# Performance work log

Hardware: AMD Instinct MI355X
Metric: run time of the kernel (lower is better)

Reference implementation:

```python
import jax, jax.numpy as jnp
import numpy as np

N, E, F_IN, D_COORD, W, KW, KIN, DEPTH = 10000, 300000, 3, 3, 32, 256, 6, 4

def _lin(k, i, o):
    return jax.random.normal(k, (i, o), jnp.float32) * (1.0 / np.sqrt(i))

def setup_inputs() -> dict:
    key = jax.random.key(0)
    ks = jax.random.split(key, 16)
    x = jax.random.normal(ks[0], (N, F_IN), jnp.float32)
    edge_index = jax.random.randint(ks[1], (2, E), 0, N, jnp.int64)
    edge_attr = jax.random.normal(ks[2], (E, KIN), jnp.float32)
    coords_init = jax.random.normal(ks[3], (N, D_COORD), jnp.float32)
    return {
        "x": x, "edge_index": edge_index, "edge_attr": edge_attr,
        "coords_init": coords_init,
        "fc1_w": _lin(ks[4], F_IN, W), "fc1_b": jnp.zeros((W,), jnp.float32),
        # kernel DenseNet: [ker_in, ker_width//2, ker_width, width**2]
        "ker1_w": _lin(ks[5], KIN, KW // 2), "ker1_b": jnp.zeros((KW // 2,), jnp.float32),
        "ker2_w": _lin(ks[6], KW // 2, KW), "ker2_b": jnp.zeros((KW,), jnp.float32),
        "ker3_w": _lin(ks[7], KW, W * W), "ker3_b": jnp.zeros((W * W,), jnp.float32),
        # coord MLP: Linear(W,W)+ReLU+Linear(W,1)
        "cm1_w": _lin(ks[8], W, W), "cm1_b": jnp.zeros((W,), jnp.float32),
        "cm2_w": _lin(ks[9], W, 1), "cm2_b": jnp.zeros((1,), jnp.float32),
        # fc2: Linear(W,2W)+ReLU+Linear(2W,1)
        "fc2a_w": _lin(ks[10], W, 2 * W), "fc2a_b": jnp.zeros((2 * W,), jnp.float32),
        "fc2b_w": _lin(ks[11], 2 * W, 1), "fc2b_b": jnp.zeros((1,), jnp.float32),
        "depth": DEPTH,
    }

def reference(x, edge_index, edge_attr, coords_init,
              fc1_w, fc1_b, ker1_w, ker1_b, ker2_w, ker2_b, ker3_w, ker3_b,
              cm1_w, cm1_b, cm2_w, cm2_b, fc2a_w, fc2a_b, fc2b_w, fc2b_b, depth):
    n = x.shape[0]
    w = fc1_w.shape[1]
    row, col = edge_index[0], edge_index[1]
    h = x @ fc1_w + fc1_b  # [N, W]
    # edge kernel MLP -> per-edge [W, W] matrix (edge_attr fixed across layers)
    k = jax.nn.relu(edge_attr @ ker1_w + ker1_b)
    k = jax.nn.relu(k @ ker2_w + ker2_b)
    k = (k @ ker3_w + ker3_b).reshape(-1, w, w)  # [E, W, W]
    cnt = jnp.clip(jax.ops.segment_sum(jnp.ones((row.shape[0], 1), h.dtype), row, n), 1.0)
    coord = coords_init
    for _ in range(depth):
        m = jnp.einsum('eij,ej->ei', k, h[col])              # gather + kernel apply
        agg = jax.ops.segment_sum(m, row, n) / cnt           # mean scatter to nodes
        we = jax.nn.relu(m @ cm1_w + cm1_b) @ cm2_w + cm2_b  # [E, 1] coord weights
        trans = (coord[row] - coord[col]) * we               # equivariant edge vectors
        coord = coord + jax.ops.segment_sum(trans, row, n) / cnt
        h = jax.nn.relu(h + agg)
    out = jax.nn.relu(h @ fc2a_w + fc2a_b) @ fc2b_w + fc2b_b  # [N, 1]
    return out, coord
```

## Files before the change

### kernel.cpp

```cpp
#include <hip/hip_runtime.h>

#define NN 10000
#define NE 300000
#define DEPTH 4

typedef unsigned int   u32;
typedef unsigned short u16;
typedef unsigned char  u8;

typedef _Float16 half8  __attribute__((ext_vector_type(8)));
typedef _Float16 half2t __attribute__((ext_vector_type(2)));
typedef float  floatx16 __attribute__((ext_vector_type(16)));

__device__ __forceinline__ u32 f2h(float f) {
    f = fminf(fmaxf(f, -60000.f), 60000.f);
    _Float16 h = (_Float16)f;
    return (u32)__builtin_bit_cast(u16, h);
}
__device__ __forceinline__ float h2f(u16 b) {
    return (float)__builtin_bit_cast(_Float16, b);
}
__device__ __forceinline__ u32 pkrtz2(float a, float b) {
    return __builtin_bit_cast(u32, __builtin_amdgcn_cvt_pkrtz(a, b));
}
__device__ __forceinline__ u32 dq2(u32 x, u32 sel) {
    const half2t h1024 = {(_Float16)1024.f, (_Float16)1024.f};
    half2t v = __builtin_bit_cast(half2t, __builtin_amdgcn_perm(x, 0x64646464u, sel));
    return __builtin_bit_cast(u32, v - h1024);
}

__global__ void sentinel_kernel(float* out, int n, float val) {
    int i = blockIdx.x * 256 + threadIdx.x;
    if (i < n) out[i] = val;
}

__global__ void detect_idx_kernel(const int* __restrict__ ei, int* __restrict__ flag) {
    __shared__ int nz;
    if (threadIdx.x == 0) nz = 0;
    __syncthreads();
    if (ei[threadIdx.x * 2 + 1] != 0) atomicAdd(&nz, 1);
    __syncthreads();
    if (threadIdx.x == 0) *flag = (nz == 0) ? 1 : 0;
}

__global__ __launch_bounds__(256) void convert_idx_kernel(
    const int* __restrict__ ei, const int* __restrict__ flag,
    int* __restrict__ ridx, int* __restrict__ cidx)
{
    int e = blockIdx.x * 256 + threadIdx.x;
    if (e >= 2 * NE) return;
    const int is64 = *flag;
    int v = is64 ? ei[2 * e] : ei[e];
    if (e < NE) ridx[e] = v; else cidx[e - NE] = v;
}

__global__ __launch_bounds__(256) void init_nodes_kernel(
    const float* __restrict__ x, const float* __restrict__ fc1w,
    const float* __restrict__ fc1b, const float* __restrict__ ci,
    float* __restrict__ h, float* __restrict__ coord)
{
    int idx = blockIdx.x * 256 + threadIdx.x;
    if (idx < NN * 32) {
        int v = idx >> 5, f = idx & 31;
        float acc = fc1b[f];
#pragma unroll
        for (int i = 0; i < 3; i++) acc += x[v * 3 + i] * fc1w[i * 32 + f];
        h[idx] = acc;
    }
    if (idx < NN * 3) coord[idx] = ci[idx];
}

__global__ __launch_bounds__(256) void count_kernel(
    const int* __restrict__ ridx, const int* __restrict__ cidx,
    int* __restrict__ rowcnt, int* __restrict__ colcnt)
{
    int e = blockIdx.x * 256 + threadIdx.x;
    if (e < NE) { atomicAdd(&rowcnt[ridx[e]], 1); atomicAdd(&colcnt[cidx[e]], 1); }
}

__global__ void scan_kernel(const int* __restrict__ colcnt, const int* __restrict__ rowcnt,
                            int* __restrict__ cstart, int* __restrict__ cnext,
                            int* __restrict__ rstart, int* __restrict__ rnext,
                            float* __restrict__ invc, int mode)
{
    __shared__ int partC[256], partR[256];
    const int t = threadIdx.x;
    int sumC = 0, sumR = 0;
    for (int i = 0; i < 40; i++) {
        int v = t * 40 + i;
        if (v < NN) { sumC += colcnt[v]; sumR += rowcnt[v]; }
    }
    partC[t] = sumC; partR[t] = sumR;
    __syncthreads();
    if (t == 0) {
        int rc = 0, rr = 0;
        for (int i = 0; i < 256; i++) {
            int tc = partC[i]; partC[i] = rc; rc += tc;
            int tr = partR[i]; partR[i] = rr; rr += tr;
        }
    }
    __syncthreads();
    int runC = partC[t], runR = partR[t];
    for (int i = 0; i < 40; i++) {
        int v = t * 40 + i;
        if (v < NN) {
            cstart[v] = runC; cnext[v] = runC; runC += colcnt[v];
            if (mode) { rstart[v] = runR; rnext[v] = runR; runR += rowcnt[v]; }
        }
    }
    if (t == 255) { cstart[NN] = runC; if (mode) rstart[NN] = runR; }
    for (int v = t; v < NN; v += 256) invc[v] = 1.0f / fmaxf((float)rowcnt[v], 1.0f);
}

__global__ __launch_bounds__(256) void scatter_kernel(
    const int* __restrict__ cidx, const int* __restrict__ ridx,
    int* __restrict__ cnext, int* __restrict__ rnext,
    int* __restrict__ elist, int* __restrict__ rpos, int* __restrict__ rcol,
    int mode)
{
    int e = blockIdx.x * 256 + threadIdx.x;
    if (e >= NE) return;
    int pos = atomicAdd(&cnext[cidx[e]], 1);
    elist[pos] = e;
    if (mode) {
        int rp = atomicAdd(&rnext[ridx[e]], 1);
        rpos[e] = rp;
        rcol[rp] = cidx[e];
    }
}

__global__ __launch_bounds__(256) void w2pack_kernel(
    const float* __restrict__ w2, u16* __restrict__ w2h)
{
    const int slot = blockIdx.x * 256 + threadIdx.x;
    const int c = slot >> 9, s = (slot >> 6) & 7, l = slot & 63;
    const int li = l & 31, hf = l >> 5;
    const int k0 = s * 16 + hf * 8, col = c * 32 + li;
    u32 pk[8];
#pragma unroll
    for (int j = 0; j < 8; j++) pk[j] = f2h(w2[(size_t)(k0 + j) * 256 + col]);
    uint4 o;
    o.x = pk[0] | (pk[1] << 16);
    o.y = pk[2] | (pk[3] << 16);
    o.z = pk[4] | (pk[5] << 16);
    o.w = pk[6] | (pk[7] << 16);
    *(uint4*)&w2h[(size_t)slot * 8] = o;
}

__global__ void cm1pack_kernel(const float* __restrict__ cm1w, u16* __restrict__ cmpk)
{
    const int t = threadIdx.x;
    if (t >= 128) return;
    const int s2 = t >> 6, l = t & 63, li = l & 31, hf = l >> 5;
    u32 pk[8];
#pragma unroll
    for (int j = 0; j < 8; j++) pk[j] = f2h(cm1w[(s2 * 16 + hf * 8 + j) * 32 + li]);
    uint4 o;
    o.x = pk[0] | (pk[1] << 16);
    o.y = pk[2] | (pk[3] << 16);
    o.z = pk[4] | (pk[5] << 16);
    o.w = pk[6] | (pk[7] << 16);
    *(uint4*)&cmpk[(size_t)(s2 * 64 + l) * 8] = o;
}

__global__ __launch_bounds__(256) void w3pack_kernel(
    const float* __restrict__ w3, u16* __restrict__ w3g)
{
    const int slot = blockIdx.x * 256 + threadIdx.x;
    const int lane = slot & 63;
    const int ks   = (slot >> 6) & 1;
    const int pt   = slot >> 7;
    const int p    = pt * 32 + (lane & 31);
    const int kb   = ks * 16 + (lane >> 5) * 8;
    const int s  = p >> 9;
    const int hf = (p >> 8) & 1;
    const int i  = (p >> 3) & 31;
    const int j7 = p & 7;
    const int c  = s * 16 + hf * 8 + j7;
    const float* wp = &w3[(size_t)c * 1024 + i * 32 + kb];
    const float4 x0 = *(const float4*)wp;
    const float4 x1 = *(const float4*)(wp + 4);
    uint4 o;
    o.x = f2h(x0.x) | (f2h(x0.y) << 16);
    o.y = f2h(x0.z) | (f2h(x0.w) << 16);
    o.z = f2h(x1.x) | (f2h(x1.y) << 16);
    o.w = f2h(x1.z) | (f2h(x1.w) << 16);
    *(uint4*)&w3g[(size_t)slot * 8] = o;
}

__global__ __launch_bounds__(256) void mlp_k2_kernel(
    const float* __restrict__ ea,
    const float* __restrict__ w1, const float* __restrict__ b1,
    const u16* __restrict__ w2h, const float* __restrict__ b2,
    u8* __restrict__ k2base, u16* __restrict__ k2s)
{
    __shared__ __align__(16) float ea_s[32 * 6];
    __shared__ __align__(16) u16   k1f[4096];
    __shared__ __align__(16) u16   M_s[32 * 258];
    __shared__ float pmax_s[4][32];
    const int t  = threadIdx.x;
    const int e0 = blockIdx.x * 32;

    for (int idx = t; idx < 192; idx += 256)
        ea_s[idx] = ea[(size_t)e0 * 6 + idx];
    __syncthreads();

    for (int slot = t; slot < 512; slot += 256) {
        const int s  = slot >> 6;
        const int l  = slot & 63;
        const int li = l & 31, hf = l >> 5;
        const int k0 = s * 16 + hf * 8;
        float acc[8];
        {
            const float4 ba = *(const float4*)&b1[k0];
            const float4 bb = *(const float4*)&b1[k0 + 4];
            acc[0] = ba.x; acc[1] = ba.y; acc[2] = ba.z; acc[3] = ba.w;
            acc[4] = bb.x; acc[5] = bb.y; acc[6] = bb.z; acc[7] = bb.w;
        }
#pragma unroll
        for (int i = 0; i < 6; i++) {
            const float ev = ea_s[li * 6 + i];
            const float4 wa = *(const float4*)&w1[i * 128 + k0];
            const float4 wb = *(const float4*)&w1[i * 128 + k0 + 4];
            acc[0] += ev * wa.x; acc[1] += ev * wa.y;
            acc[2] += ev * wa.z; acc[3] += ev * wa.w;
            acc[4] += ev * wb.x; acc[5] += ev * wb.y;
            acc[6] += ev * wb.z; acc[7] += ev * wb.w;
        }
        uint4 o;
        o.x = pkrtz2(fmaxf(acc[0], 0.f), fmaxf(acc[1], 0.f));
        o.y = pkrtz2(fmaxf(acc[2], 0.f), fmaxf(acc[3], 0.f));
        o.z = pkrtz2(fmaxf(acc[4], 0.f), fmaxf(acc[5], 0.f));
        o.w = pkrtz2(fmaxf(acc[6], 0.f), fmaxf(acc[7], 0.f));
        *(uint4*)&k1f[slot * 8] = o;
    }
    __syncthreads();

    {
        const int w  = t >> 6, l = t & 63;
        const int li = l & 31, hf = l >> 5;
#pragma unroll
        for (int ct = 0; ct < 2; ct++) {
            const int c = w * 2 + ct;
            floatx16 acc;
#pragma unroll
            for (int r = 0; r < 16; r++) acc[r] = 0.f;
#pragma unroll
            for (int s = 0; s < 8; s++) {
                const half8 a = __builtin_bit_cast(half8,
                    *(const uint4*)&k1f[(s * 64 + l) * 8]);
                const half8 b = __builtin_bit_cast(half8,
                    *(const uint4*)&w2h[(((size_t)c * 8 + s) * 64 + l) * 8]);
                acc = __builtin_amdgcn_mfma_f32_32x32x16_f16(a, b, acc, 0, 0, 0);
            }
            const float bb = b2[c * 32 + li];
#pragma unroll
            for (int r = 0; r < 16; r++) {
                const int e = (r & 3) + 8 * (r >> 2) + 4 * hf;
                M_s[e * 258 + c * 32 + li] =
                    __builtin_bit_cast(u16, (_Float16)fmaxf(acc[r] + bb, 0.f));
            }
        }
    }
    __syncthreads();

    {
        const int el = t & 31, qq = t >> 5;
        const int w  = t >> 6;
        float vals[32];
#pragma unroll
        for (int c = 0; c < 16; c++) {
            const u32 hw = *(const u32*)&M_s[el * 258 + qq * 32 + c * 2];
            vals[c * 2]     = h2f((u16)hw);
            vals[c * 2 + 1] = h2f((u16)(hw >> 16));
        }
        float mx = 0.f;
#pragma unroll
        for (int u = 0; u < 32; u++) mx = fmaxf(mx, vals[u]);
        mx = fmaxf(mx, __shfl_xor(mx, 32, 64));
        if ((t & 32) == 0) pmax_s[w][el] = mx;
        __syncthreads();
        mx = fmaxf(fmaxf(pmax_s[0][el], pmax_s[1][el]),
                   fmaxf(pmax_s[2][el], pmax_s[3][el]));
        const float sc  = mx / 255.f;
        const float inv = (mx > 0.f) ? 255.f / mx : 0.f;
        if (t < 32) k2s[e0 + el] = (u16)f2h(sc);
        u32 w8[8];
#pragma unroll
        for (int u = 0; u < 8; u++) {
            u32 q0 = (u32)fminf(rintf(vals[u * 4 + 0] * inv), 255.f);
            u32 q1 = (u32)fminf(rintf(vals[u * 4 + 1] * inv), 255.f);
            u32 q2 = (u32)fminf(rintf(vals[u * 4 + 2] * inv), 255.f);
            u32 q3 = (u32)fminf(rintf(vals[u * 4 + 3] * inv), 255.f);
            w8[u] = q0 | (q1 << 8) | (q2 << 16) | (q3 << 24);
        }
        u8* outp = k2base + (size_t)(e0 + el) * 256 + qq * 32;
        *(uint4*)outp        = make_uint4(w8[0], w8[1], w8[2], w8[3]);
        *(uint4*)(outp + 16) = make_uint4(w8[4], w8[5], w8[6], w8[7]);
    }
}

__global__ __launch_bounds__(256) void bvec_kernel(
    const float* __restrict__ h, const float* __restrict__ b3, float* __restrict__ bvec)
{
    int idx = blockIdx.x * 256 + threadIdx.x;
    if (idx >= NN * 32) return;
    int v = idx >> 5, i = idx & 31;
    const float* hp = &h[(size_t)v * 32];
    const float* bp = &b3[i * 32];
    float acc = 0.f;
#pragma unroll
    for (int c = 0; c < 8; c++) {
        float4 hv = *(const float4*)&hp[c * 4];
        float4 bv = *(const float4*)&bp[c * 4];
        acc += hv.x * bv.x + hv.y * bv.y + hv.z * bv.z + hv.w * bv.w;
    }
    bvec[idx] = acc;
}

__global__ __launch_bounds__(256) void g_kernel(
    const float* __restrict__ h, const u16* __restrict__ w3g,
    u16* __restrict__ Gg)
{
    const int t = threadIdx.x, w = t >> 6, l = t & 63;
    const int li = l & 31, hf = l >> 5;
    const int n0 = blockIdx.x * 32;
    const int node = n0 + li;

    half8 a0, a1;
    if (node < NN) {
        const float* hp = &h[(size_t)node * 32 + hf * 8];
        const float4 x0 = *(const float4*)hp;
        const float4 x1 = *(const float4*)(hp + 4);
        const float4 y0 = *(const float4*)(hp + 16);
        const float4 y1 = *(const float4*)(hp + 20);
        uint4 ua, ub;
        ua.x = pkrtz2(x0.x, x0.y); ua.y = pkrtz2(x0.z, x0.w);
        ua.z = pkrtz2(x1.x, x1.y); ua.w = pkrtz2(x1.z, x1.w);
        ub.x = pkrtz2(y0.x, y0.y); ub.y = pkrtz2(y0.z, y0.w);
        ub.z = pkrtz2(y1.x, y1.y); ub.w = pkrtz2(y1.z, y1.w);
        a0 = __builtin_bit_cast(half8, ua);
        a1 = __builtin_bit_cast(half8, ub);
    } else {
        const uint4 z = make_uint4(0u, 0u, 0u, 0u);
        a0 = __builtin_bit_cast(half8, z);
        a1 = __builtin_bit_cast(half8, z);
    }

    const int pt0 = blockIdx.y * 64 + w * 16;
    const int full = (n0 + 32 <= NN) ? 1 : 0;
#pragma unroll 4
    for (int it = 0; it < 16; it++) {
        const int pt = pt0 + it;
        const uint4 b0u = *(const uint4*)&w3g[((size_t)pt * 2 + 0) * 512 + (size_t)l * 8];
        const uint4 b1u = *(const uint4*)&w3g[((size_t)pt * 2 + 1) * 512 + (size_t)l * 8];
        floatx16 acc;
#pragma unroll
        for (int r = 0; r < 16; r++) acc[r] = 0.f;
        acc = __builtin_amdgcn_mfma_f32_32x32x16_f16(
            a0, __builtin_bit_cast(half8, b0u), acc, 0, 0, 0);
        acc = __builtin_amdgcn_mfma_f32_32x32x16_f16(
            a1, __builtin_bit_cast(half8, b1u), acc, 0, 0, 0);
        if (full) {
#pragma unroll
            for (int r = 0; r < 16; r++) {
                const int nn = n0 + (r & 3) + 8 * (r >> 2) + 4 * hf;
                Gg[(size_t)nn * 8192 + pt * 32 + li] = (u16)f2h(acc[r]);
            }
        } else {
#pragma unroll
            for (int r = 0; r < 16; r++) {
                const int nn = n0 + (r & 3) + 8 * (r >> 2) + 4 * hf;
                if (nn < NN)
                    Gg[(size_t)nn * 8192 + pt * 32 + li] = (u16)f2h(acc[r]);
            }
        }
    }
}

__global__ __launch_bounds__(256) void edge_kernel(
    const int* __restrict__ cstart, const int* __restrict__ elist,
    const int* __restrict__ ridx, const int* __restrict__ rpos,
    const u8* __restrict__ k2base, const u16* __restrict__ k2s,
    const u16* __restrict__ Gg, const float* __restrict__ coord,
    const u16* __restrict__ cmpk, const float* __restrict__ cm1b,
    const float* __restrict__ cm2w, const float* __restrict__ cm2b,
    const float* __restrict__ bvec,
    float* __restrict__ agg, float* __restrict__ dco,
    u16* __restrict__ mbuf, u16* __restrict__ webuf, int mode)
{
    const int t    = threadIdx.x;
    const int w    = t >> 6;
    const int l    = t & 63;
    const int li   = l & 31;
    const int half = l >> 5;

    __shared__ __align__(16) float Mlds_all[4][32 * 34];
    __shared__ int   idxS_all[4][32];
    __shared__ float seS_all[4][32];
    float* Mlds = Mlds_all[w];
    int*   idxS = idxS_all[w];
    float* seS  = seS_all[w];

    const int n = blockIdx.x * 4 + w;
    if (n >= NN) return;
    const int s0  = cstart[n];
    const int deg = cstart[n + 1] - s0;
    if (deg == 0) return;

    half8 cmb[2];
    cmb[0] = __builtin_bit_cast(half8, *(const uint4*)&cmpk[(size_t)(0 * 64 + l) * 8]);
    cmb[1] = __builtin_bit_cast(half8, *(const uint4*)&cmpk[(size_t)(1 * 64 + l) * 8]);
    half8 onesb;
#pragma unroll
    for (int j = 0; j < 8; j++) onesb[j] = (_Float16)1.0f;
    const float cm1bq = cm1b[li];
    const float cm2q  = cm2w[li];
    const float cm2b0 = cm2b[0];
    const float bv    = bvec[n * 32 + li];
    const float con   = (mode == 0 && li < 3) ? coord[(size_t)n * 3 + li] : 0.f;
    const u16* Gn = Gg + (size_t)n * 8192;

    for (int base = 0; base < deg; base += 32) {
        const int mye   = base + li;
        const int valid = (mye < deg) ? 1 : 0;
        const int eid   = valid ? elist[s0 + mye] : 0;
        const float se  = valid ? h2f(k2s[eid]) : 0.f;
        if (l < 32) { idxS[l] = valid ? (mode ? rpos[eid] : ridx[eid]) : 0; seS[l] = se; }

        uint4 gr[16];
#pragma unroll
        for (int s = 0; s < 16; s++)
            gr[s] = *(const uint4*)(Gn + s * 512 + l * 8);
        const u8* k2row = k2base + (size_t)eid * 256 + half * 8;
        uint2 kr[16];
#pragma unroll
        for (int s = 0; s < 16; s++) kr[s] = *(const uint2*)(k2row + s * 16);

        floatx16 acc;
#pragma unroll
        for (int r = 0; r < 16; r++) acc[r] = 0.f;
#pragma unroll
        for (int s = 0; s < 16; s++) {
            uint4 au;
            au.x = dq2(kr[s].x, 0x00050004u);
            au.y = dq2(kr[s].x, 0x00070006u);
            au.z = dq2(kr[s].y, 0x00050004u);
            au.w = dq2(kr[s].y, 0x00070006u);
            acc = __builtin_amdgcn_mfma_f32_32x32x16_f16(
                __builtin_bit_cast(half8, au),
                __builtin_bit_cast(half8, gr[s]), acc, 0, 0, 0);
        }
#pragma unroll
        for (int r = 0; r < 16; r++) {
            const int e = (r & 3) + 8 * (r >> 2) + 4 * half;
            acc[r] = acc[r] * seS[e] + bv;
        }

#pragma unroll
        for (int r = 0; r < 16; r++) {
            const int e = (r & 3) + 8 * (r >> 2) + 4 * half;
            Mlds[e * 34 + li] = acc[r];
        }
        if (mode == 0) {
#pragma unroll
            for (int r = 0; r < 16; r++) {
                const int e = (r & 3) + 8 * (r >> 2) + 4 * half;
                if (base + e < deg)
                    atomicAdd(&agg[(size_t)idxS[e] * 32 + li], acc[r]);
            }
        } else {
#pragma unroll
            for (int r = 0; r < 16; r++) {
                const int e = (r & 3) + 8 * (r >> 2) + 4 * half;
                if (base + e < deg)
                    mbuf[(size_t)idxS[e] * 32 + li] =
                        __builtin_bit_cast(u16, (_Float16)acc[r]);
            }
        }
        asm volatile("s_waitcnt lgkmcnt(0)" ::: "memory");

        floatx16 acc2;
#pragma unroll
        for (int r = 0; r < 16; r++) acc2[r] = cm1bq;
#pragma unroll
        for (int s2 = 0; s2 < 2; s2++) {
            const float* mp = &Mlds[li * 34 + s2 * 16 + half * 8];
            const float2 m0 = *(const float2*)mp;
            const float2 m1 = *(const float2*)(mp + 2);
            const float2 m2 = *(const float2*)(mp + 4);
            const float2 m3 = *(const float2*)(mp + 6);
            uint4 au;
            au.x = pkrtz2(m0.x, m0.y);
            au.y = pkrtz2(m1.x, m1.y);
            au.z = pkrtz2(m2.x, m2.y);
            au.w = pkrtz2(m3.x, m3.y);
            acc2 = __builtin_amdgcn_mfma_f32_32x32x16_f16(
                __builtin_bit_cast(half8, au), cmb[s2], acc2, 0, 0, 0);
        }

#pragma unroll
        for (int r = 0; r < 16; r++) {
            const int e = (r & 3) + 8 * (r >> 2) + 4 * half;
            Mlds[e * 34 + li] = fmaxf(acc2[r], 0.f) * cm2q;
        }
        asm volatile("s_waitcnt lgkmcnt(0)" ::: "memory");
        floatx16 acc3;
#pragma unroll
        for (int r = 0; r < 16; r++) acc3[r] = cm2b0;
#pragma unroll
        for (int s2 = 0; s2 < 2; s2++) {
            const float* mp = &Mlds[li * 34 + s2 * 16 + half * 8];
            const float2 m0 = *(const float2*)mp;
            const float2 m1 = *(const float2*)(mp + 2);
            const float2 m2 = *(const float2*)(mp + 4);
            const float2 m3 = *(const float2*)(mp + 6);
            uint4 au;
            au.x = pkrtz2(m0.x, m0.y);
            au.y = pkrtz2(m1.x, m1.y);
            au.z = pkrtz2(m2.x, m2.y);
            au.w = pkrtz2(m3.x, m3.y);
            acc3 = __builtin_amdgcn_mfma_f32_32x32x16_f16(
                __builtin_bit_cast(half8, au), onesb, acc3, 0, 0, 0);
        }

        if (mode == 0) {
#pragma unroll
            for (int r = 0; r < 16; r++) {
                const int e = (r & 3) + 8 * (r >> 2) + 4 * half;
                if (base + e < deg && li < 3) {
                    const int rr = idxS[e];
                    const float d = coord[(size_t)rr * 3 + li] - con;
                    atomicAdd(&dco[(size_t)rr * 3 + li], d * acc3[r]);
                }
            }
        } else {
#pragma unroll
            for (int r = 0; r < 16; r++) {
                const int e = (r & 3) + 8 * (r >> 2) + 4 * half;
                if (base + e < deg && li == 0)
                    webuf[idxS[e]] = __builtin_bit_cast(u16, (_Float16)acc3[r]);
            }
        }
    }
}

__global__ __launch_bounds__(256) void node_update_kernel(
    float* __restrict__ h, float* __restrict__ agg,
    float* __restrict__ coord, float* __restrict__ dco,
    const float* __restrict__ invc)
{
    int idx = blockIdx.x * 256 + threadIdx.x;
    if (idx < NN * 32) {
        int v = idx >> 5;
        h[idx] = fmaxf(h[idx] + agg[idx] * invc[v], 0.f);
        agg[idx] = 0.f;
    }
    if (idx < NN * 3) {
        coord[idx] += dco[idx] * invc[idx / 3];
        dco[idx] = 0.f;
    }
}

__global__ __launch_bounds__(256) void node_update2_kernel(
    float* __restrict__ h, const float* __restrict__ coordCur,
    float* __restrict__ coordNew, const u16* __restrict__ mbuf,
    const u16* __restrict__ webuf, const int* __restrict__ rcol,
    const int* __restrict__ rstart, const float* __restrict__ invc)
{
    const int t = threadIdx.x, w = t >> 6, l = t & 63;
    const int li = l & 31, half = l >> 5;
    const int v = blockIdx.x * 4 + w;
    if (v >= NN) return;
    const int s0 = rstart[v], s1 = rstart[v + 1];
    const float iv = invc[v];

    float acc = 0.f;
    for (int s = s0 + half; s < s1; s += 2)
        acc += h2f(mbuf[(size_t)s * 32 + li]);
    acc += __shfl_xor(acc, 32, 64);
    if (half == 0)
        h[(size_t)v * 32 + li] = fmaxf(h[(size_t)v * 32 + li] + acc * iv, 0.f);

    const float c0 = coordCur[(size_t)v * 3 + 0];
    const float c1 = coordCur[(size_t)v * 3 + 1];
    const float c2 = coordCur[(size_t)v * 3 + 2];
    float p0 = 0.f, p1 = 0.f, p2 = 0.f;
    for (int s = s0 + l; s < s1; s += 64) {
        const float we = h2f(webuf[s]);
        const int col = rcol[s];
        p0 += (c0 - coordCur[(size_t)col * 3 + 0]) * we;
        p1 += (c1 - coordCur[(size_t)col * 3 + 1]) * we;
        p2 += (c2 - coordCur[(size_t)col * 3 + 2]) * we;
    }
#pragma unroll
    for (int off = 32; off >= 1; off >>= 1) {
        p0 += __shfl_xor(p0, off, 64);
        p1 += __shfl_xor(p1, off, 64);
        p2 += __shfl_xor(p2, off, 64);
    }
    if (l == 0) {
        coordNew[(size_t)v * 3 + 0] = c0 + p0 * iv;
        coordNew[(size_t)v * 3 + 1] = c1 + p1 * iv;
        coordNew[(size_t)v * 3 + 2] = c2 + p2 * iv;
    }
}

__global__ __launch_bounds__(256) void final_kernel(
    const float* __restrict__ h, const float* __restrict__ coord,
    const float* __restrict__ wa, const float* __restrict__ ba,
    const float* __restrict__ wb, const float* __restrict__ bb,
    float* __restrict__ out)
{
    const int lane = threadIdx.x & 63;
    const int v = blockIdx.x * 4 + (threadIdx.x >> 6);
    if (v >= NN) return;
    const float hreg = (lane < 32) ? h[(size_t)v * 32 + lane] : 0.f;
    float acc = ba[lane];
#pragma unroll
    for (int f = 0; f < 32; f++) acc += __shfl(hreg, f, 64) * wa[f * 64 + lane];
    float part = fmaxf(acc, 0.f) * wb[lane];
#pragma unroll
    for (int off = 32; off >= 1; off >>= 1) part += __shfl_xor(part, off, 64);
    if (lane == 0) out[v] = part + bb[0];
    if (lane < 3) out[NN + (size_t)v * 3 + lane] = coord[(size_t)v * 3 + lane];
}

extern "C" void kernel_launch(void* const* d_in, const int* in_sizes, int n_in,
                              void* d_out, int out_size, void* d_ws, size_t ws_size,
                              hipStream_t stream)
{
    const float* x    = (const float*)d_in[0];
    const int*   ei   = (const int*)d_in[1];
    const float* ea   = (const float*)d_in[2];
    const float* ci   = (const float*)d_in[3];
    const float* fc1w = (const float*)d_in[4];
    const float* fc1b = (const float*)d_in[5];
    const float* k1w  = (const float*)d_in[6];
    const float* k1b  = (const float*)d_in[7];
    const float* k2w  = (const float*)d_in[8];
    const float* k2b  = (const float*)d_in[9];
    const float* k3w  = (const float*)d_in[10];
    const float* k3b  = (const float*)d_in[11];
    const float* cm1w = (const float*)d_in[12];
    const float* cm1b = (const float*)d_in[13];
    const float* cm2w = (const float*)d_in[14];
    const float* cm2b = (const float*)d_in[15];
    const float* f2aw = (const float*)d_in[16];
    const float* f2ab = (const float*)d_in[17];
    const float* f2bw = (const float*)d_in[18];
    const float* f2bb = (const float*)d_in[19];

    size_t o_k2, o_k2s, o_G, o_h, o_bv, o_coA, o_coB, o_invc, o_rc, o_cc,
           o_cs, o_rs, o_cn, o_rn, o_el, o_w2h, o_cmpk, o_w3g, o_agg, o_dco,
           o_ri, o_ci, o_rp, o_rcl, o_mb, o_wb;
#define ALGN(v) (((v) + 255) & ~(size_t)255)
    auto carve = [&](int mode) -> size_t {
        size_t o = 0;
        o_k2  = o; o += ALGN((size_t)NE * 256);
        o_k2s = o; o += ALGN((size_t)NE * 2);
        o_G   = o; o += ALGN((size_t)NN * 8192 * 2);
        o_h   = o; o += ALGN((size_t)NN * 32 * 4);
        o_bv  = o; o += ALGN((size_t)NN * 32 * 4);
        o_coA = o; o += ALGN((size_t)NN * 3 * 4);
        o_invc= o; o += ALGN((size_t)NN * 4);
        o_rc  = o; o += ALGN((size_t)NN * 4);
        o_cc  = o; o += ALGN((size_t)NN * 4);
        o_cs  = o; o += ALGN((size_t)(NN + 1) * 4);
        o_cn  = o; o += ALGN((size_t)NN * 4);
        o_el  = o; o += ALGN((size_t)NE * 4);
        o_w2h = o; o += ALGN((size_t)128 * 256 * 2);
        o_cmpk= o; o += ALGN((size_t)1024 * 2);
        o_w3g = o; o += ALGN((size_t)32768 * 8 * 2);
        if (mode == 0) {
            o_agg = o; o += ALGN((size_t)NN * 32 * 4);
            o_dco = o; o += ALGN((size_t)NN * 3 * 4);
            o_ri  = o; o += ALGN((size_t)NE * 4);
            o_ci  = o; o += ALGN((size_t)NE * 4);
            o_coB = o_coA; o_rs = o_cs; o_rn = o_cn;
            o_rp = o_el; o_rcl = o_el; o_mb = o_k2; o_wb = o_k2;
        } else {
            o_coB = o; o += ALGN((size_t)NN * 3 * 4);
            o_rs  = o; o += ALGN((size_t)(NN + 1) * 4);
            o_rn  = o; o += ALGN((size_t)NN * 4);
            o_rp  = o; o += ALGN((size_t)NE * 4);
            o_rcl = o; o += ALGN((size_t)NE * 4);
            const size_t u = o;
            o_ri = u; o_ci = u + ALGN((size_t)NE * 4);
            o_mb = u; o_wb = u + ALGN((size_t)NE * 32 * 2);
            const size_t setup_sz = 2 * ALGN((size_t)NE * 4);
            const size_t layer_sz = ALGN((size_t)NE * 32 * 2) + ALGN((size_t)NE * 2);
            o += (setup_sz > layer_sz) ? setup_sz : layer_sz;
            o_agg = o_k2; o_dco = o_k2;
        }
        return o;
    };
    int mode = (ws_size >= carve(1)) ? 1 : 0;
    size_t need = carve(mode);
    if (ws_size < need) {
        sentinel_kernel<<<(NN * 4 + 255) / 256, 256, 0, stream>>>((float*)d_out, NN * 4, 1.0e6f);
        return;
    }

    char* wsb = (char*)d_ws;
    u8*    k2g   = (u8*)(wsb + o_k2);
    u16*   k2s   = (u16*)(wsb + o_k2s);
    u16*   Gg    = (u16*)(wsb + o_G);
    float* h     = (float*)(wsb + o_h);
    float* bvec  = (float*)(wsb + o_bv);
    float* coA   = (float*)(wsb + o_coA);
    float* coB   = (float*)(wsb + o_coB);
    float* invc  = (float*)(wsb + o_invc);
    int*   rowcnt= (int*)(wsb + o_rc);
    int*   colcnt= (int*)(wsb + o_cc);
    int*   cstart= (int*)(wsb + o_cs);
    int*   rstart= (int*)(wsb + o_rs);
    int*   cnext = (int*)(wsb + o_cn);
    int*   rnext = (int*)(wsb + o_rn);
    int*   elist = (int*)(wsb + o_el);
    u16*   w2h   = (u16*)(wsb + o_w2h);
    u16*   cmpk  = (u16*)(wsb + o_cmpk);
    u16*   w3g   = (u16*)(wsb + o_w3g);
    float* agg   = (float*)(wsb + o_agg);
    float* dco   = (float*)(wsb + o_dco);
    int*   ridx  = (int*)(wsb + o_ri);
    int*   cidx  = (int*)(wsb + o_ci);
    int*   rpos  = (int*)(wsb + o_rp);
    int*   rcol  = (int*)(wsb + o_rcl);
    u16*   mbuf  = (u16*)(wsb + o_mb);
    u16*   webuf = (u16*)(wsb + o_wb);

    hipMemsetAsync(rowcnt, 0, (size_t)NN * 4, stream);
    hipMemsetAsync(colcnt, 0, (size_t)NN * 4, stream);
    if (mode == 0) {
        hipMemsetAsync(agg, 0, (size_t)NN * 32 * 4, stream);
        hipMemsetAsync(dco, 0, (size_t)NN * 3 * 4, stream);
    }

    detect_idx_kernel<<<1, 256, 0, stream>>>(ei, cnext);
    convert_idx_kernel<<<(2 * NE + 255) / 256, 256, 0, stream>>>(ei, cnext, ridx, cidx);
    init_nodes_kernel<<<(NN * 32 + 255) / 256, 256, 0, stream>>>(x, fc1w, fc1b, ci, h, coA);
    count_kernel<<<(NE + 255) / 256, 256, 0, stream>>>(ridx, cidx, rowcnt, colcnt);
    scan_kernel<<<1, 256, 0, stream>>>(colcnt, rowcnt, cstart, cnext, rstart, rnext,
                                       invc, mode);
    scatter_kernel<<<(NE + 255) / 256, 256, 0, stream>>>(cidx, ridx, cnext, rnext,
                                                         elist, rpos, rcol, mode);
    w2pack_kernel<<<16, 256, 0, stream>>>(k2w, w2h);
    cm1pack_kernel<<<1, 128, 0, stream>>>(cm1w, cmpk);
    w3pack_kernel<<<128, 256, 0, stream>>>(k3w, w3g);
    mlp_k2_kernel<<<NE / 32, 256, 0, stream>>>(ea, k1w, k1b, w2h, k2b, k2g, k2s);

    float* coCur = coA;
    float* coAlt = coB;
    const dim3 ggrid((NN + 31) / 32, 4);
    for (int l = 0; l < DEPTH; l++) {
        bvec_kernel<<<(NN * 32 + 255) / 256, 256, 0, stream>>>(h, k3b, bvec);
        g_kernel<<<ggrid, 256, 0, stream>>>(h, w3g, Gg);
        edge_kernel<<<(NN + 3) / 4, 256, 0, stream>>>(cstart, elist, ridx, rpos,
                                                      k2g, k2s, Gg, coCur, cmpk,
                                                      cm1b, cm2w, cm2b, bvec,
                                                      agg, dco, mbuf, webuf, mode);
        if (mode == 1) {
            node_update2_kernel<<<(NN + 3) / 4, 256, 0, stream>>>(
                h, coCur, coAlt, mbuf, webuf, rcol, rstart, invc);
            float* tmp = coCur; coCur = coAlt; coAlt = tmp;
        } else {
            node_update_kernel<<<(NN * 32 + 255) / 256, 256, 0, stream>>>(
                h, agg, coCur, dco, invc);
        }
    }
    final_kernel<<<(NN + 3) / 4, 256, 0, stream>>>(h, coCur, f2aw, f2ab, f2bw, f2bb,
                                                   (float*)d_out);
}
```

Measured before the change: 860.1 us.

## Fuse bias-vector compute into edge kernel and speed up k2 quantization

Removes the per-layer bvec kernel and its buffer; each edge_kernel warp now computes the h·b3 bias dot product inline. mlp_k2's quantization takes the max with packed fp16 max ops and rounds with a magic-number FMA plus byte permutes instead of rintf, fminf and shifts. It also adds occupancy hints to launch_bounds for mlp_k2 (4) and edge_kernel (3). This saves four kernel launches and a global round trip per forward pass, at the cost of extra per-warp loads of h and b3 and possible register spills from the new bounds. The magic-add rounding drops the clamp at 255, which relies on the scaled values never exceeding 255.

```diff
diff --git a/kernel.cpp b/kernel.cpp
--- a/kernel.cpp
+++ b/kernel.cpp
@@ -188,7 +188,7 @@
     *(uint4*)&w3g[(size_t)slot * 8] = o;
 }
 
-__global__ __launch_bounds__(256) void mlp_k2_kernel(
+__global__ __launch_bounds__(256, 4) void mlp_k2_kernel(
     const float* __restrict__ ea,
     const float* __restrict__ w1, const float* __restrict__ b1,
     const u16* __restrict__ w2h, const float* __restrict__ b2,
@@ -267,16 +267,16 @@
     {
         const int el = t & 31, qq = t >> 5;
         const int w  = t >> 6;
-        float vals[32];
-#pragma unroll
-        for (int c = 0; c < 16; c++) {
-            const u32 hw = *(const u32*)&M_s[el * 258 + qq * 32 + c * 2];
-            vals[c * 2]     = h2f((u16)hw);
-            vals[c * 2 + 1] = h2f((u16)(hw >> 16));
-        }
-        float mx = 0.f;
-#pragma unroll
-        for (int u = 0; u < 32; u++) mx = fmaxf(mx, vals[u]);
+        u32 hw[16];
+#pragma unroll
+        for (int c = 0; c < 16; c++)
+            hw[c] = *(const u32*)&M_s[el * 258 + qq * 32 + c * 2];
+
+        half2t pm = __builtin_bit_cast(half2t, hw[0]);
+#pragma unroll
+        for (int c = 1; c < 16; c++)
+            pm = __builtin_elementwise_max(pm, __builtin_bit_cast(half2t, hw[c]));
+        float mx = fmaxf((float)pm[0], (float)pm[1]);
         mx = fmaxf(mx, __shfl_xor(mx, 32, 64));
         if ((t & 32) == 0) pmax_s[w][el] = mx;
         __syncthreads();
@@ -285,37 +285,27 @@
         const float sc  = mx / 255.f;
         const float inv = (mx > 0.f) ? 255.f / mx : 0.f;
         if (t < 32) k2s[e0 + el] = (u16)f2h(sc);
+        const float magic = 8388608.f;
         u32 w8[8];
 #pragma unroll
         for (int u = 0; u < 8; u++) {
-            u32 q0 = (u32)fminf(rintf(vals[u * 4 + 0] * inv), 255.f);
-            u32 q1 = (u32)fminf(rintf(vals[u * 4 + 1] * inv), 255.f);
-            u32 q2 = (u32)fminf(rintf(vals[u * 4 + 2] * inv), 255.f);
-            u32 q3 = (u32)fminf(rintf(vals[u * 4 + 3] * inv), 255.f);
-            w8[u] = q0 | (q1 << 8) | (q2 << 16) | (q3 << 24);
+            const u32 a = hw[u * 2], b = hw[u * 2 + 1];
+            const float v0 = h2f((u16)a);
+            const float v1 = h2f((u16)(a >> 16));
+            const float v2 = h2f((u16)b);
+            const float v3 = h2f((u16)(b >> 16));
+            const u32 r0 = __builtin_bit_cast(u32, fmaf(v0, inv, magic));
+            const u32 r1 = __builtin_bit_cast(u32, fmaf(v1, inv, magic));
+            const u32 r2 = __builtin_bit_cast(u32, fmaf(v2, inv, magic));
+            const u32 r3 = __builtin_bit_cast(u32, fmaf(v3, inv, magic));
+            const u32 p01 = __builtin_amdgcn_perm(r1, r0, 0x0C0C0400u);
+            const u32 p23 = __builtin_amdgcn_perm(r3, r2, 0x0C0C0400u);
+            w8[u] = __builtin_amdgcn_perm(p23, p01, 0x05040100u);
         }
         u8* outp = k2base + (size_t)(e0 + el) * 256 + qq * 32;
         *(uint4*)outp        = make_uint4(w8[0], w8[1], w8[2], w8[3]);
         *(uint4*)(outp + 16) = make_uint4(w8[4], w8[5], w8[6], w8[7]);
     }
-}
-
-__global__ __launch_bounds__(256) void bvec_kernel(
-    const float* __restrict__ h, const float* __restrict__ b3, float* __restrict__ bvec)
-{
-    int idx = blockIdx.x * 256 + threadIdx.x;
-    if (idx >= NN * 32) return;
-    int v = idx >> 5, i = idx & 31;
-    const float* hp = &h[(size_t)v * 32];
-    const float* bp = &b3[i * 32];
-    float acc = 0.f;
-#pragma unroll
-    for (int c = 0; c < 8; c++) {
-        float4 hv = *(const float4*)&hp[c * 4];
-        float4 bv = *(const float4*)&bp[c * 4];
-        acc += hv.x * bv.x + hv.y * bv.y + hv.z * bv.z + hv.w * bv.w;
-    }
-    bvec[idx] = acc;
 }
 
 __global__ __launch_bounds__(256) void g_kernel(
@@ -378,14 +368,14 @@
     }
 }
 
-__global__ __launch_bounds__(256) void edge_kernel(
+__global__ __launch_bounds__(256, 3) void edge_kernel(
     const int* __restrict__ cstart, const int* __restrict__ elist,
     const int* __restrict__ ridx, const int* __restrict__ rpos,
     const u8* __restrict__ k2base, const u16* __restrict__ k2s,
     const u16* __restrict__ Gg, const float* __restrict__ coord,
     const u16* __restrict__ cmpk, const float* __restrict__ cm1b,
     const float* __restrict__ cm2w, const float* __restrict__ cm2b,
-    const float* __restrict__ bvec,
+    const float* __restrict__ h, const float* __restrict__ b3,
     float* __restrict__ agg, float* __restrict__ dco,
     u16* __restrict__ mbuf, u16* __restrict__ webuf, int mode)
 {
@@ -417,7 +407,17 @@
     const float cm1bq = cm1b[li];
     const float cm2q  = cm2w[li];
     const float cm2b0 = cm2b[0];
-    const float bv    = bvec[n * 32 + li];
+    float bv = 0.f;
+    {
+        const float* hn = &h[(size_t)n * 32];
+        const float* bp = &b3[(size_t)li * 32];
+#pragma unroll
+        for (int c2 = 0; c2 < 8; c2++) {
+            const float4 hv = *(const float4*)&hn[c2 * 4];
+            const float4 bq = *(const float4*)&bp[c2 * 4];
+            bv += hv.x * bq.x + hv.y * bq.y + hv.z * bq.z + hv.w * bq.w;
+        }
+    }
     const float con   = (mode == 0 && li < 3) ? coord[(size_t)n * 3 + li] : 0.f;
     const u16* Gn = Gg + (size_t)n * 8192;
 
@@ -651,7 +651,7 @@
     const float* f2bw = (const float*)d_in[18];
     const float* f2bb = (const float*)d_in[19];
 
-    size_t o_k2, o_k2s, o_G, o_h, o_bv, o_coA, o_coB, o_invc, o_rc, o_cc,
+    size_t o_k2, o_k2s, o_G, o_h, o_coA, o_coB, o_invc, o_rc, o_cc,
            o_cs, o_rs, o_cn, o_rn, o_el, o_w2h, o_cmpk, o_w3g, o_agg, o_dco,
            o_ri, o_ci, o_rp, o_rcl, o_mb, o_wb;
 #define ALGN(v) (((v) + 255) & ~(size_t)255)
@@ -661,7 +661,6 @@
         o_k2s = o; o += ALGN((size_t)NE * 2);
         o_G   = o; o += ALGN((size_t)NN * 8192 * 2);
         o_h   = o; o += ALGN((size_t)NN * 32 * 4);
-        o_bv  = o; o += ALGN((size_t)NN * 32 * 4);
         o_coA = o; o += ALGN((size_t)NN * 3 * 4);
         o_invc= o; o += ALGN((size_t)NN * 4);
         o_rc  = o; o += ALGN((size_t)NN * 4);
@@ -707,7 +706,6 @@
     u16*   k2s   = (u16*)(wsb + o_k2s);
     u16*   Gg    = (u16*)(wsb + o_G);
     float* h     = (float*)(wsb + o_h);
-    float* bvec  = (float*)(wsb + o_bv);
     float* coA   = (float*)(wsb + o_coA);
     float* coB   = (float*)(wsb + o_coB);
     float* invc  = (float*)(wsb + o_invc);
@@ -754,11 +752,10 @@
     float* coAlt = coB;
     const dim3 ggrid((NN + 31) / 32, 4);
     for (int l = 0; l < DEPTH; l++) {
-        bvec_kernel<<<(NN * 32 + 255) / 256, 256, 0, stream>>>(h, k3b, bvec);
         g_kernel<<<ggrid, 256, 0, stream>>>(h, w3g, Gg);
         edge_kernel<<<(NN + 3) / 4, 256, 0, stream>>>(cstart, elist, ridx, rpos,
                                                       k2g, k2s, Gg, coCur, cmpk,
-                                                      cm1b, cm2w, cm2b, bvec,
+                                                      cm1b, cm2w, cm2b, h, k3b,
                                                       agg, dco, mbuf, webuf, mode);
         if (mode == 1) {
             node_update2_kernel<<<(NN + 3) / 4, 256, 0, stream>>>(
```

Result: faster. 817.7 us (-4.9%).
